# Kernel tuning notes

Measured on AMD Instinct MI355X. Metric: run time of the kernel, lower is better.

Reference implementation:

```python
import jax, jax.numpy as jnp
import numpy as np

IMAGE_SIZE = 512


def setup_inputs() -> dict:
    key = jax.random.key(0)
    k1, k2, k3, k4, k5 = jax.random.split(key, 5)
    B, S, C, P = 64, IMAGE_SIZE, 64, IMAGE_SIZE * IMAGE_SIZE
    x = jax.random.normal(k1, (B, S, S), dtype=jnp.float32)
    pattern_importance = jax.random.uniform(k2, (B, C), dtype=jnp.float32)
    idxx = jax.random.randint(k3, (P,), 0, S)
    idxy = jax.random.randint(k4, (P,), 0, S)
    cluster_id = jax.random.randint(k5, (P,), 0, C)
    return {"x": x, "pattern_importance": pattern_importance,
            "idxx": idxx, "idxy": idxy, "cluster_id": cluster_id}


def reference(x, pattern_importance, idxx, idxy, cluster_id):
    S = IMAGE_SIZE
    # fft2 with zero-pad/crop to (S, S), then shift DC to center
    x_fft = jnp.fft.fftshift(jnp.fft.fft2(x, s=(S, S), axes=(-2, -1)), axes=(-2, -1))
    # mask: ones everywhere, per-cluster importance scattered at clustered freq bins
    B = x.shape[0]
    mask = jnp.ones((B, S, S), dtype=x.dtype)
    # mask[j, idxx, idxy] = pattern_importance[j, cluster_id] for all batches j at once
    mask = mask.at[:, idxx, idxy].set(pattern_importance[:, cluster_id])
    x_reject = x_fft * mask
    x_ifft = jnp.real(jnp.fft.ifft2(jnp.fft.ifftshift(x_reject, axes=(-2, -1)),
                                    s=(x.shape[1], x.shape[2]), axes=(-2, -1)))
    return x_ifft
```

## Files before the change

### kernel.cpp

```cpp
#include <hip/hip_runtime.h>

#define INV_N2 (1.0f/262144.0f)
#define HALF_INV (0.5f*INV_N2)
#define TP 17
#define YT_B ((size_t)(264 * 512))

typedef unsigned u32x2 __attribute__((ext_vector_type(2)));
typedef float v2f __attribute__((ext_vector_type(2)));

__device__ __forceinline__ v2f v2(float a, float b) { v2f r; r.x = a; r.y = b; return r; }
__device__ __forceinline__ int brev9(int v) { return (int)(__brev((unsigned)v) >> 23); }
__device__ __forceinline__ float hsin(float rev) { return __builtin_amdgcn_sinf(rev); }
__device__ __forceinline__ float hcos(float rev) { return __builtin_amdgcn_cosf(rev); }

template<int CTRL>
__device__ __forceinline__ float xdpp(float x) {
  int v = __float_as_int(x);
  return __int_as_float(__builtin_amdgcn_update_dpp(v, v, CTRL, 0xF, 0xF, true));
}
__device__ __forceinline__ float xs1(float x) { return xdpp<0xB1>(x); }
__device__ __forceinline__ float xs2(float x) { return xdpp<0x4E>(x); }
__device__ __forceinline__ float xs8(float x) { return xdpp<0x128>(x); }
__device__ __forceinline__ float xs4(float x) {
  return __int_as_float(__builtin_amdgcn_ds_swizzle(__float_as_int(x), 0x101F));
}
__device__ __forceinline__ void swp16(float x, float &lo, float &hi) {
#if __has_builtin(__builtin_amdgcn_permlane16_swap)
  u32x2 r = __builtin_amdgcn_permlane16_swap(__float_as_uint(x), __float_as_uint(x), false, false);
  lo = __uint_as_float(r[0]); hi = __uint_as_float(r[1]);
#else
  float p = __int_as_float(__builtin_amdgcn_ds_swizzle(__float_as_int(x), 0x401F));
  bool up = (threadIdx.x & 16) != 0;
  lo = up ? p : x; hi = up ? x : p;
#endif
}
__device__ __forceinline__ void swp32(float x, float &lo, float &hi) {
#if __has_builtin(__builtin_amdgcn_permlane32_swap)
  u32x2 r = __builtin_amdgcn_permlane32_swap(__float_as_uint(x), __float_as_uint(x), false, false);
  lo = __uint_as_float(r[0]); hi = __uint_as_float(r[1]);
#else
  float p = __shfl_xor(x, 32, 64);
  bool up = (threadIdx.x & 32) != 0;
  lo = up ? p : x; hi = up ? x : p;
#endif
}

struct Tw { float c[8], s[8]; };
__device__ __forceinline__ Tw make_tw(int lane) {
  Tw t;
  float a0 = (float)lane        * (1.0f/512.0f);
  float a1 = (float)lane        * (1.0f/256.0f);
  float a2 = (float)lane        * (1.0f/128.0f);
  float a3 = (float)(lane & 31) * (1.0f/64.0f);
  float a4 = (float)(lane & 15) * (1.0f/32.0f);
  float a5 = (float)(lane & 7)  * (1.0f/16.0f);
  float a6 = (float)(lane & 3)  * (1.0f/8.0f);
  float a7 = (float)(lane & 1)  * (1.0f/4.0f);
  t.c[0]=hcos(a0); t.s[0]=hsin(a0); t.c[1]=hcos(a1); t.s[1]=hsin(a1);
  t.c[2]=hcos(a2); t.s[2]=hsin(a2); t.c[3]=hcos(a3); t.s[3]=hsin(a3);
  t.c[4]=hcos(a4); t.s[4]=hsin(a4); t.c[5]=hcos(a5); t.s[5]=hsin(a5);
  t.c[6]=hcos(a6); t.s[6]=hsin(a6); t.c[7]=hcos(a7); t.s[7]=hsin(a7);
  return t;
}

#define FWD_PK_XS(S, XCHG, CC, SS) { \
  const bool up = (lane & (S)) != 0; \
  const float sg = up ? -1.0f : 1.0f; \
  const float wr = up ? (CC) : 1.0f; \
  const float wi = up ? -(SS) : 0.0f; \
  const v2f sgv = v2(sg,sg), wrv = v2(wr,wr), wiv = v2(wi,wi); \
  _Pragma("unroll") for (int j = 0; j < 4; ++j) { \
    v2f Rr = v2(XCHG(Xr[j].x), XCHG(Xr[j].y)); \
    v2f Ri = v2(XCHG(Xi[j].x), XCHG(Xi[j].y)); \
    v2f vr = sgv*Xr[j] + Rr; v2f vi = sgv*Xi[j] + Ri; \
    Xr[j] = vr*wrv - vi*wiv; Xi[j] = vr*wiv + vi*wrv; } }

#define FWD_PK_SW(S, SWP, CC, SS) { \
  const bool up = (lane & (S)) != 0; \
  const float sg = up ? -1.0f : 1.0f; \
  const float wr = up ? (CC) : 1.0f; \
  const float wi = up ? -(SS) : 0.0f; \
  const v2f sgv = v2(sg,sg), wrv = v2(wr,wr), wiv = v2(wi,wi); \
  _Pragma("unroll") for (int j = 0; j < 4; ++j) { \
    float l0,h0,l1,h1; \
    SWP(Xr[j].x,l0,h0); SWP(Xr[j].y,l1,h1); \
    v2f Lr = v2(l0,l1), Hr = v2(h0,h1); \
    SWP(Xi[j].x,l0,h0); SWP(Xi[j].y,l1,h1); \
    v2f Li = v2(l0,l1), Hi = v2(h0,h1); \
    v2f vr = sgv*Hr + Lr; v2f vi = sgv*Hi + Li; \
    Xr[j] = vr*wrv - vi*wiv; Xi[j] = vr*wiv + vi*wrv; } }

#define INV_PK_XS(S, XCHG, CC, SS) { \
  const bool up = (lane & (S)) != 0; \
  const float wr = up ? (CC) : 1.0f; \
  const float wi = up ? (SS) : 0.0f; \
  const float sg = up ? -1.0f : 1.0f; \
  const v2f sgv = v2(sg,sg), wrv = v2(wr,wr), wiv = v2(wi,wi); \
  _Pragma("unroll") for (int j = 0; j < 4; ++j) { \
    v2f Zr = Xr[j]*wrv - Xi[j]*wiv; \
    v2f Zi = Xr[j]*wiv + Xi[j]*wrv; \
    v2f Rr = v2(XCHG(Zr.x), XCHG(Zr.y)); \
    v2f Ri = v2(XCHG(Zi.x), XCHG(Zi.y)); \
    Xr[j] = sgv*Zr + Rr; Xi[j] = sgv*Zi + Ri; } }

#define INV_PK_SW(S, SWP, CC, SS) { \
  const bool up = (lane & (S)) != 0; \
  const float wr = up ? (CC) : 1.0f; \
  const float wi = up ? (SS) : 0.0f; \
  const float sg = up ? -1.0f : 1.0f; \
  const v2f sgv = v2(sg,sg), wrv = v2(wr,wr), wiv = v2(wi,wi); \
  _Pragma("unroll") for (int j = 0; j < 4; ++j) { \
    v2f Zr = Xr[j]*wrv - Xi[j]*wiv; \
    v2f Zi = Xr[j]*wiv + Xi[j]*wrv; \
    float l0,h0,l1,h1; \
    SWP(Zr.x,l0,h0); SWP(Zr.y,l1,h1); \
    v2f Lr = v2(l0,l1), Hr = v2(h0,h1); \
    SWP(Zi.x,l0,h0); SWP(Zi.y,l1,h1); \
    v2f Li = v2(l0,l1), Hi = v2(h0,h1); \
    Xr[j] = sgv*Hr + Lr; Xi[j] = sgv*Hi + Li; } }

__device__ __forceinline__ void wave_fft512_fwd(v2f Xr[4], v2f Xi[4], int lane,
                                                const Tw& t) {
  {
    const float c8 = 0.70710678118654752f;
    float wr = t.c[0], wi = -t.s[0];
    float w1r = c8*(wr + wi), w1i = c8*(wi - wr);
    v2f Tr0 = v2(wr, w1r), Ti0 = v2(wi, w1i);
    { v2f Sr = Xr[0]+Xr[2], Si = Xi[0]+Xi[2];
      v2f Dr = Xr[0]-Xr[2], Di = Xi[0]-Xi[2];
      Xr[0] = Sr; Xi[0] = Si;
      Xr[2] = Dr*Tr0 - Di*Ti0; Xi[2] = Dr*Ti0 + Di*Tr0; }
    { v2f Sr = Xr[1]+Xr[3], Si = Xi[1]+Xi[3];
      v2f Dr = Xr[1]-Xr[3], Di = Xi[1]-Xi[3];
      Xr[1] = Sr; Xi[1] = Si;
      Xr[3] = Dr*Ti0 + Di*Tr0; Xi[3] = Di*Ti0 - Dr*Tr0; }
  }
  {
    v2f Tr = v2(t.c[1], -t.s[1]), Ti = v2(-t.s[1], -t.c[1]);
    #pragma unroll
    for (int j = 0; j < 4; j += 2) {
      v2f Sr = Xr[j]+Xr[j+1], Si = Xi[j]+Xi[j+1];
      v2f Dr = Xr[j]-Xr[j+1], Di = Xi[j]-Xi[j+1];
      Xr[j] = Sr; Xi[j] = Si;
      Xr[j+1] = Dr*Tr - Di*Ti; Xi[j+1] = Dr*Ti + Di*Tr;
    }
  }
  {
    float wr = t.c[2], wi = -t.s[2];
    #pragma unroll
    for (int j = 0; j < 4; ++j) {
      float sr = Xr[j].x + Xr[j].y, si = Xi[j].x + Xi[j].y;
      float dr = Xr[j].x - Xr[j].y, di = Xi[j].x - Xi[j].y;
      Xr[j] = v2(sr, dr*wr - di*wi);
      Xi[j] = v2(si, dr*wi + di*wr);
    }
  }
  FWD_PK_SW(32, swp32, t.c[3], t.s[3])
  FWD_PK_SW(16, swp16, t.c[4], t.s[4])
  FWD_PK_XS(8,  xs8,  t.c[5], t.s[5])
  FWD_PK_XS(4,  xs4,  t.c[6], t.s[6])
  FWD_PK_XS(2,  xs2,  t.c[7], t.s[7])
  {
    const float sg = (lane & 1) ? -1.0f : 1.0f;
    const v2f sgv = v2(sg, sg);
    #pragma unroll
    for (int j = 0; j < 4; ++j) {
      v2f Rr = v2(xs1(Xr[j].x), xs1(Xr[j].y));
      v2f Ri = v2(xs1(Xi[j].x), xs1(Xi[j].y));
      Xr[j] = sgv*Xr[j] + Rr; Xi[j] = sgv*Xi[j] + Ri;
    }
  }
}

__device__ __forceinline__ void wave_fft512_inv(v2f Xr[4], v2f Xi[4], int lane,
                                                const Tw& t) {
  {
    const float sg = (lane & 1) ? -1.0f : 1.0f;
    const v2f sgv = v2(sg, sg);
    #pragma unroll
    for (int j = 0; j < 4; ++j) {
      v2f Rr = v2(xs1(Xr[j].x), xs1(Xr[j].y));
      v2f Ri = v2(xs1(Xi[j].x), xs1(Xi[j].y));
      Xr[j] = sgv*Xr[j] + Rr; Xi[j] = sgv*Xi[j] + Ri;
    }
  }
  INV_PK_XS(2,  xs2,  t.c[7], t.s[7])
  INV_PK_XS(4,  xs4,  t.c[6], t.s[6])
  INV_PK_XS(8,  xs8,  t.c[5], t.s[5])
  INV_PK_SW(16, swp16, t.c[4], t.s[4])
  INV_PK_SW(32, swp32, t.c[3], t.s[3])
  {
    float wr = t.c[2], wi = t.s[2];
    #pragma unroll
    for (int j = 0; j < 4; ++j) {
      float tr = Xr[j].y*wr - Xi[j].y*wi, ti = Xr[j].y*wi + Xi[j].y*wr;
      Xr[j] = v2(Xr[j].x + tr, Xr[j].x - tr);
      Xi[j] = v2(Xi[j].x + ti, Xi[j].x - ti);
    }
  }
  {
    v2f Tr = v2(t.c[1], -t.s[1]), Ti = v2(t.s[1], t.c[1]);
    #pragma unroll
    for (int j = 0; j < 4; j += 2) {
      v2f tr = Xr[j+1]*Tr - Xi[j+1]*Ti;
      v2f ti = Xr[j+1]*Ti + Xi[j+1]*Tr;
      Xr[j+1] = Xr[j] - tr; Xi[j+1] = Xi[j] - ti;
      Xr[j]   = Xr[j] + tr; Xi[j]   = Xi[j] + ti;
    }
  }
  {
    const float c8 = 0.70710678118654752f;
    float wr = t.c[0], wi = t.s[0];
    float w1r = c8*(wr - wi), w1i = c8*(wr + wi);
    v2f Tr0 = v2(wr, w1r), Ti0 = v2(wi, w1i);
    { v2f tr = Xr[2]*Tr0 - Xi[2]*Ti0;
      v2f ti = Xr[2]*Ti0 + Xi[2]*Tr0;
      Xr[2] = Xr[0] - tr; Xi[2] = Xi[0] - ti;
      Xr[0] = Xr[0] + tr; Xi[0] = Xi[0] + ti; }
    { v2f tr = Xr[3]*Tr0 + Xi[3]*Ti0;
      v2f ti = Xr[3]*Tr0 - Xi[3]*Ti0;
      tr = -(Xr[3]*Ti0) - Xi[3]*Tr0;
      ti = Xr[3]*Tr0 - Xi[3]*Ti0;
      Xr[3] = Xr[1] - tr; Xi[3] = Xi[1] - ti;
      Xr[1] = Xr[1] + tr; Xi[1] = Xi[1] + ti; }
  }
}

__global__ void k_scatter(const int* __restrict__ idxx, const int* __restrict__ idxy,
                          const int* __restrict__ cid, int* __restrict__ W) {
  int p = blockIdx.x * 256 + threadIdx.x;
  int u = (idxx[p] + 256) & 511;
  int v = (idxy[p] + 256) & 511;
  atomicMax(&W[u * 512 + v], (p << 6) | cid[p]);
}

__global__ void k_pack(const int* __restrict__ W, int* __restrict__ pk) {
  int idx = blockIdx.x * 256 + threadIdx.x;
  if (idx >= 264 * 512) return;
  int j = idx >> 9, n = idx & 511;
  int out = (127 << 7) | 127;
  if (j < 257) {
    int v = (j == 256) ? 256 : brev9(2 * j);
    int u = brev9(n);
    int c1 = W[u * 512 + v];
    int c2 = W[((512 - u) & 511) * 512 + ((512 - v) & 511)];
    int a = (c1 < 0) ? 127 : (c1 & 63);
    int b = (c2 < 0) ? 127 : (c2 & 63);
    out = (b << 7) | a;
  }
  pk[j * 512 + n] = out;
}

__global__ __launch_bounds__(512) void k_fwd_rows(const float* __restrict__ x,
                                                  float2* __restrict__ Yt) {
  __shared__ float sm[2 * 264 * TP];
  float* tR = sm;
  float* tI = sm + 264 * TP;
  int tid = threadIdx.x, w = tid >> 6, lane = tid & 63;
  int R0 = blockIdx.x * 16;
  int bb = R0 >> 9, r0 = R0 & 511;
  const float* rowA = x + (size_t)(R0 + 2 * w) * 512;
  const float* rowB = rowA + 512;
  Tw t = make_tw(lane);
  v2f Xr[4], Xi[4];
  #pragma unroll
  for (int j = 0; j < 4; ++j) {
    Xr[j] = v2(rowA[(2*j)*64 + lane], rowA[(2*j+1)*64 + lane]);
    Xi[j] = v2(rowB[(2*j)*64 + lane], rowB[(2*j+1)*64 + lane]);
  }
  wave_fft512_fwd(Xr, Xi, lane, t);
  float* zr = sm + w * 1024;
  float* zi = zr + 512;
  #pragma unroll
  for (int j = 0; j < 4; ++j) {
    zr[(2*j)*64 + lane] = Xr[j].x; zr[(2*j+1)*64 + lane] = Xr[j].y;
    zi[(2*j)*64 + lane] = Xi[j].x; zi[(2*j+1)*64 + lane] = Xi[j].y;
  }
  float ar[4], ai[4], br[4], bi[4];
  #pragma unroll
  for (int k = 0; k < 4; ++k) {
    int j = k * 64 + lane;
    int n2 = 2 * j;
    int kf = brev9(n2);
    int m = brev9((512 - kf) & 511);
    float er = zr[n2], ei = zi[n2];
    float mr = zr[m],  mi = zi[m];
    ar[k] = 0.5f * (er + mr); ai[k] = 0.5f * (ei - mi);
    br[k] = 0.5f * (ei + mi); bi[k] = 0.5f * (mr - er);
  }
  float a256 = zr[1], b256 = zi[1];
  __syncthreads();
  #pragma unroll
  for (int k = 0; k < 4; ++k) {
    int j = k * 64 + lane;
    tR[j*TP + 2*w]     = ar[k]; tI[j*TP + 2*w]     = ai[k];
    tR[j*TP + 2*w + 1] = br[k]; tI[j*TP + 2*w + 1] = bi[k];
  }
  if (lane == 0) {
    tR[256*TP + 2*w]     = a256; tI[256*TP + 2*w]     = 0.0f;
    tR[256*TP + 2*w + 1] = b256; tI[256*TP + 2*w + 1] = 0.0f;
  }
  __syncthreads();
  #pragma unroll
  for (int rep = 0; rep < 9; ++rep) {
    int e = rep * 512 + tid;
    int j = e >> 4, rr = e & 15;
    if (j < 257)
      Yt[((size_t)bb * 264 + j) * 512 + r0 + rr] =
        make_float2(tR[j*TP + rr], tI[j*TP + rr]);
  }
}

__global__ __launch_bounds__(512) void k_cols(float2* __restrict__ Yt,
                                              const int* __restrict__ pk,
                                              const float* __restrict__ pimp) {
  __shared__ float pilx[128];
  int tid = threadIdx.x;
  int b = blockIdx.x / 33, g = blockIdx.x % 33;
  if (tid < 128) pilx[tid] = (tid < 64) ? pimp[b * 64 + tid] * HALF_INV : HALF_INV;
  int w = tid >> 6, lane = tid & 63;
  int j = g * 8 + w;
  float2* col = Yt + ((size_t)b * 264 + j) * 512;
  const int* cm = pk + j * 512;
  int pcm[8];
  v2f Xr[4], Xi[4];
  #pragma unroll
  for (int q = 0; q < 4; ++q) {
    float2 v0 = col[(2*q)*64 + lane];
    float2 v1 = col[(2*q+1)*64 + lane];
    Xr[q] = v2(v0.x, v1.x); Xi[q] = v2(v0.y, v1.y);
    pcm[2*q]   = cm[(2*q)*64 + lane];
    pcm[2*q+1] = cm[(2*q+1)*64 + lane];
  }
  Tw t = make_tw(lane);
  wave_fft512_fwd(Xr, Xi, lane, t);
  __syncthreads();
  #pragma unroll
  for (int q = 0; q < 4; ++q) {
    int p0 = pcm[2*q], p1 = pcm[2*q+1];
    v2f mv = v2(pilx[p0 & 127] + pilx[(p0 >> 7) & 127],
                pilx[p1 & 127] + pilx[(p1 >> 7) & 127]);
    Xr[q] *= mv; Xi[q] *= mv;
  }
  wave_fft512_inv(Xr, Xi, lane, t);
  #pragma unroll
  for (int q = 0; q < 4; ++q) {
    col[(2*q)*64 + lane]   = make_float2(Xr[q].x, Xi[q].x);
    col[(2*q+1)*64 + lane] = make_float2(Xr[q].y, Xi[q].y);
  }
}

__global__ __launch_bounds__(512) void k_inv_rows(const float2* __restrict__ Yt,
                                                  float* __restrict__ out) {
  __shared__ float tR[264 * TP], tI[264 * TP];
  int tid = threadIdx.x, w = tid >> 6, lane = tid & 63;
  int R0 = blockIdx.x * 16;
  int bb = R0 >> 9, r0 = R0 & 511;
  #pragma unroll
  for (int rep = 0; rep < 9; ++rep) {
    int e = rep * 512 + tid;
    int j = e >> 4, rr = e & 15;
    if (j < 257) {
      float2 v = Yt[((size_t)bb * 264 + j) * 512 + r0 + rr];
      tR[j*TP + rr] = v.x; tI[j*TP + rr] = v.y;
    }
  }
  Tw t = make_tw(lane);
  __syncthreads();
  v2f Xr[4], Xi[4];
  #pragma unroll
  for (int q = 0; q < 4; ++q) {
    float xr2[2], xi2[2];
    #pragma unroll
    for (int h = 0; h < 2; ++h) {
      int n = (2*q + h) * 64 + lane;
      int v9 = brev9(n);
      int j2 = brev9((512 - v9) & 511) >> 1;
      bool oddx = (n & 1) && (n != 1);
      int j = (n & 1) ? ((n == 1) ? 256 : j2) : (n >> 1);
      float s = oddx ? -1.0f : 1.0f;
      float ar = tR[j*TP + 2*w],     ai = tI[j*TP + 2*w];
      float br = tR[j*TP + 2*w + 1], bi = tI[j*TP + 2*w + 1];
      xr2[h] = ar - s * bi;
      xi2[h] = fmaf(s, ai, br);
    }
    Xr[q] = v2(xr2[0], xr2[1]); Xi[q] = v2(xi2[0], xi2[1]);
  }
  wave_fft512_inv(Xr, Xi, lane, t);
  float* orowA = out + (size_t)(R0 + 2 * w) * 512;
  float* orowB = orowA + 512;
  #pragma unroll
  for (int q = 0; q < 4; ++q) {
    orowA[(2*q)*64 + lane]   = Xr[q].x;
    orowA[(2*q+1)*64 + lane] = Xr[q].y;
    orowB[(2*q)*64 + lane]   = Xi[q].x;
    orowB[(2*q+1)*64 + lane] = Xi[q].y;
  }
}

extern "C" void kernel_launch(void* const* d_in, const int* in_sizes, int n_in,
                              void* d_out, int out_size, void* d_ws, size_t ws_size,
                              hipStream_t stream) {
  const float* x    = (const float*)d_in[0];
  const float* pimp = (const float*)d_in[1];
  const int* idxx   = (const int*)d_in[2];
  const int* idxy   = (const int*)d_in[3];
  const int* cid    = (const int*)d_in[4];

  float2* Yt = (float2*)d_ws;
  int* W  = (int*)((char*)d_ws + (size_t)64 * YT_B * sizeof(float2));
  int* pk = W + 512 * 512;

  hipMemsetAsync(W, 0xFF, 512 * 512 * sizeof(int), stream);
  k_scatter  <<<1024, 256, 0, stream>>>(idxx, idxy, cid, W);
  k_pack     <<<(264 * 512 + 255) / 256, 256, 0, stream>>>(W, pk);
  k_fwd_rows <<<2048, 512, 0, stream>>>(x, Yt);
  k_cols     <<<64 * 33, 512, 0, stream>>>(Yt, pk, pimp);
  k_inv_rows <<<2048, 512, 0, stream>>>(Yt, (float*)d_out);
}
```

Before: 199.8 us.

## Emit inverse-row inputs in blocked layout from column kernel, simplify inverse rows

The column FFT kernel now does the real-pair unpacking (using cross-lane swaps) itself and writes its results to a second buffer. That buffer uses a row-group-blocked layout already indexed by the target frequency. The inverse row kernel can then load contiguous float4 tiles and read its inputs straight from shared memory, without the bit-reverse index computation and the strided gather. This is meant to cut uncoalesced global reads and ALU work in the last stage, at the cost of scattered 8-byte writes in the column kernel and a separate workspace region.

```diff
diff --git a/kernel.cpp b/kernel.cpp
--- a/kernel.cpp
+++ b/kernel.cpp
@@ -4,6 +4,7 @@
 #define HALF_INV (0.5f*INV_N2)
 #define TP 17
 #define YT_B ((size_t)(264 * 512))
+#define Y2N 520
 
 typedef unsigned u32x2 __attribute__((ext_vector_type(2)));
 typedef float v2f __attribute__((ext_vector_type(2)));
@@ -217,10 +218,8 @@
       v2f ti = Xr[2]*Ti0 + Xi[2]*Tr0;
       Xr[2] = Xr[0] - tr; Xi[2] = Xi[0] - ti;
       Xr[0] = Xr[0] + tr; Xi[0] = Xi[0] + ti; }
-    { v2f tr = Xr[3]*Tr0 + Xi[3]*Ti0;
+    { v2f tr = -(Xr[3]*Ti0) - Xi[3]*Tr0;
       v2f ti = Xr[3]*Tr0 - Xi[3]*Ti0;
-      tr = -(Xr[3]*Ti0) - Xi[3]*Tr0;
-      ti = Xr[3]*Tr0 - Xi[3]*Ti0;
       Xr[3] = Xr[1] - tr; Xi[3] = Xi[1] - ti;
       Xr[1] = Xr[1] + tr; Xi[1] = Xi[1] + ti; }
   }
@@ -311,7 +310,8 @@
   }
 }
 
-__global__ __launch_bounds__(512) void k_cols(float2* __restrict__ Yt,
+__global__ __launch_bounds__(512) void k_cols(const float2* __restrict__ Yt,
+                                              float2* __restrict__ Yt2,
                                               const int* __restrict__ pk,
                                               const float* __restrict__ pimp) {
   __shared__ float pilx[128];
@@ -320,7 +320,7 @@
   if (tid < 128) pilx[tid] = (tid < 64) ? pimp[b * 64 + tid] * HALF_INV : HALF_INV;
   int w = tid >> 6, lane = tid & 63;
   int j = g * 8 + w;
-  float2* col = Yt + ((size_t)b * 264 + j) * 512;
+  const float2* col = Yt + ((size_t)b * 264 + j) * 512;
   const int* cm = pk + j * 512;
   int pcm[8];
   v2f Xr[4], Xi[4];
@@ -343,51 +343,54 @@
     Xr[q] *= mv; Xi[q] *= mv;
   }
   wave_fft512_inv(Xr, Xi, lane, t);
-  #pragma unroll
-  for (int q = 0; q < 4; ++q) {
-    col[(2*q)*64 + lane]   = make_float2(Xr[q].x, Xi[q].x);
-    col[(2*q+1)*64 + lane] = make_float2(Xr[q].y, Xi[q].y);
-  }
-}
-
-__global__ __launch_bounds__(512) void k_inv_rows(const float2* __restrict__ Yt,
+  if (j <= 256) {
+    int n_e = (j == 256) ? 1 : 2 * j;
+    int n_o = (j >= 1 && j <= 255) ? brev9(512 - brev9(2 * j)) : 513;
+    bool odd = (lane & 1) != 0;
+    int nsel = odd ? n_o : n_e;
+    int rpb = b * 256 + (lane >> 1);
+    #pragma unroll
+    for (int q = 0; q < 4; ++q) {
+      #pragma unroll
+      for (int h = 0; h < 2; ++h) {
+        float xr = h ? Xr[q].y : Xr[q].x;
+        float xi = h ? Xi[q].y : Xi[q].x;
+        float p  = xr - xs1(xi);
+        float s2 = xi + xs1(xr);
+        float ox = odd ? s2 : p;
+        float oy = odd ? p  : s2;
+        int rp = rpb + (2*q + h) * 32;
+        Yt2[((size_t)(rp >> 3) * Y2N + nsel) * 8 + (rp & 7)] = make_float2(ox, oy);
+      }
+    }
+  }
+}
+
+__global__ __launch_bounds__(512) void k_inv_rows(const float2* __restrict__ Yt2,
                                                   float* __restrict__ out) {
-  __shared__ float tR[264 * TP], tI[264 * TP];
+  __shared__ float tR[512 * 9], tI[512 * 9];
   int tid = threadIdx.x, w = tid >> 6, lane = tid & 63;
-  int R0 = blockIdx.x * 16;
-  int bb = R0 >> 9, r0 = R0 & 511;
-  #pragma unroll
-  for (int rep = 0; rep < 9; ++rep) {
-    int e = rep * 512 + tid;
-    int j = e >> 4, rr = e & 15;
-    if (j < 257) {
-      float2 v = Yt[((size_t)bb * 264 + j) * 512 + r0 + rr];
-      tR[j*TP + rr] = v.x; tI[j*TP + rr] = v.y;
-    }
+  int g = blockIdx.x;
+  const float4* src = (const float4*)(Yt2 + (size_t)g * Y2N * 8);
+  #pragma unroll
+  for (int rep = 0; rep < 4; ++rep) {
+    int m = rep * 512 + tid;
+    int n = m >> 2, c = m & 3;
+    float4 v = src[m];
+    tR[n*9 + 2*c]     = v.x; tI[n*9 + 2*c]     = v.y;
+    tR[n*9 + 2*c + 1] = v.z; tI[n*9 + 2*c + 1] = v.w;
   }
   Tw t = make_tw(lane);
   __syncthreads();
   v2f Xr[4], Xi[4];
   #pragma unroll
   for (int q = 0; q < 4; ++q) {
-    float xr2[2], xi2[2];
-    #pragma unroll
-    for (int h = 0; h < 2; ++h) {
-      int n = (2*q + h) * 64 + lane;
-      int v9 = brev9(n);
-      int j2 = brev9((512 - v9) & 511) >> 1;
-      bool oddx = (n & 1) && (n != 1);
-      int j = (n & 1) ? ((n == 1) ? 256 : j2) : (n >> 1);
-      float s = oddx ? -1.0f : 1.0f;
-      float ar = tR[j*TP + 2*w],     ai = tI[j*TP + 2*w];
-      float br = tR[j*TP + 2*w + 1], bi = tI[j*TP + 2*w + 1];
-      xr2[h] = ar - s * bi;
-      xi2[h] = fmaf(s, ai, br);
-    }
-    Xr[q] = v2(xr2[0], xr2[1]); Xi[q] = v2(xi2[0], xi2[1]);
+    int n0 = (2*q)*64 + lane, n1 = (2*q+1)*64 + lane;
+    Xr[q] = v2(tR[n0*9 + w], tR[n1*9 + w]);
+    Xi[q] = v2(tI[n0*9 + w], tI[n1*9 + w]);
   }
   wave_fft512_inv(Xr, Xi, lane, t);
-  float* orowA = out + (size_t)(R0 + 2 * w) * 512;
+  float* orowA = out + (size_t)(g * 16 + 2 * w) * 512;
   float* orowB = orowA + 512;
   #pragma unroll
   for (int q = 0; q < 4; ++q) {
@@ -410,11 +413,12 @@
   float2* Yt = (float2*)d_ws;
   int* W  = (int*)((char*)d_ws + (size_t)64 * YT_B * sizeof(float2));
   int* pk = W + 512 * 512;
+  float2* Yt2 = (float2*)((char*)d_ws + (size_t)72 * 1024 * 1024);
 
   hipMemsetAsync(W, 0xFF, 512 * 512 * sizeof(int), stream);
   k_scatter  <<<1024, 256, 0, stream>>>(idxx, idxy, cid, W);
   k_pack     <<<(264 * 512 + 255) / 256, 256, 0, stream>>>(W, pk);
   k_fwd_rows <<<2048, 512, 0, stream>>>(x, Yt);
-  k_cols     <<<64 * 33, 512, 0, stream>>>(Yt, pk, pimp);
-  k_inv_rows <<<2048, 512, 0, stream>>>(Yt, (float*)d_out);
-}
+  k_cols     <<<64 * 33, 512, 0, stream>>>(Yt, Yt2, pk, pimp);
+  k_inv_rows <<<2048, 512, 0, stream>>>(Yt2, (float*)d_out);
+}
```

After: 209.9 us. +5.0%, slower.

## Process two FFT lines per wave with 256-thread blocks

Applied to the files above, without the earlier changes.

Each wavefront now runs two 512-point FFTs at once (eight packed registers instead of four), and the blocks in the row, column and inverse-row kernels shrink from 512 to 256 threads while covering the same rows or columns. The aim is more instruction-level parallelism per wave and amortised twiddle setup and cross-lane exchange, with fewer waves per block. The cost is higher register pressure, which may lower occupancy, and each remaining thread does more of the shared-memory transpose traffic.

```diff
diff --git a/kernel.cpp b/kernel.cpp
--- a/kernel.cpp
+++ b/kernel.cpp
@@ -69,7 +69,7 @@
   const float wr = up ? (CC) : 1.0f; \
   const float wi = up ? -(SS) : 0.0f; \
   const v2f sgv = v2(sg,sg), wrv = v2(wr,wr), wiv = v2(wi,wi); \
-  _Pragma("unroll") for (int j = 0; j < 4; ++j) { \
+  _Pragma("unroll") for (int j = 0; j < 8; ++j) { \
     v2f Rr = v2(XCHG(Xr[j].x), XCHG(Xr[j].y)); \
     v2f Ri = v2(XCHG(Xi[j].x), XCHG(Xi[j].y)); \
     v2f vr = sgv*Xr[j] + Rr; v2f vi = sgv*Xi[j] + Ri; \
@@ -81,7 +81,7 @@
   const float wr = up ? (CC) : 1.0f; \
   const float wi = up ? -(SS) : 0.0f; \
   const v2f sgv = v2(sg,sg), wrv = v2(wr,wr), wiv = v2(wi,wi); \
-  _Pragma("unroll") for (int j = 0; j < 4; ++j) { \
+  _Pragma("unroll") for (int j = 0; j < 8; ++j) { \
     float l0,h0,l1,h1; \
     SWP(Xr[j].x,l0,h0); SWP(Xr[j].y,l1,h1); \
     v2f Lr = v2(l0,l1), Hr = v2(h0,h1); \
@@ -96,7 +96,7 @@
   const float wi = up ? (SS) : 0.0f; \
   const float sg = up ? -1.0f : 1.0f; \
   const v2f sgv = v2(sg,sg), wrv = v2(wr,wr), wiv = v2(wi,wi); \
-  _Pragma("unroll") for (int j = 0; j < 4; ++j) { \
+  _Pragma("unroll") for (int j = 0; j < 8; ++j) { \
     v2f Zr = Xr[j]*wrv - Xi[j]*wiv; \
     v2f Zi = Xr[j]*wiv + Xi[j]*wrv; \
     v2f Rr = v2(XCHG(Zr.x), XCHG(Zr.y)); \
@@ -109,7 +109,7 @@
   const float wi = up ? (SS) : 0.0f; \
   const float sg = up ? -1.0f : 1.0f; \
   const v2f sgv = v2(sg,sg), wrv = v2(wr,wr), wiv = v2(wi,wi); \
-  _Pragma("unroll") for (int j = 0; j < 4; ++j) { \
+  _Pragma("unroll") for (int j = 0; j < 8; ++j) { \
     v2f Zr = Xr[j]*wrv - Xi[j]*wiv; \
     v2f Zi = Xr[j]*wiv + Xi[j]*wrv; \
     float l0,h0,l1,h1; \
@@ -119,26 +119,29 @@
     v2f Li = v2(l0,l1), Hi = v2(h0,h1); \
     Xr[j] = sgv*Hr + Lr; Xi[j] = sgv*Hi + Li; } }
 
-__device__ __forceinline__ void wave_fft512_fwd(v2f Xr[4], v2f Xi[4], int lane,
-                                                const Tw& t) {
+__device__ __forceinline__ void wave_fft512_fwd2(v2f Xr[8], v2f Xi[8], int lane,
+                                                 const Tw& t) {
   {
     const float c8 = 0.70710678118654752f;
     float wr = t.c[0], wi = -t.s[0];
     float w1r = c8*(wr + wi), w1i = c8*(wi - wr);
     v2f Tr0 = v2(wr, w1r), Ti0 = v2(wi, w1i);
-    { v2f Sr = Xr[0]+Xr[2], Si = Xi[0]+Xi[2];
-      v2f Dr = Xr[0]-Xr[2], Di = Xi[0]-Xi[2];
-      Xr[0] = Sr; Xi[0] = Si;
-      Xr[2] = Dr*Tr0 - Di*Ti0; Xi[2] = Dr*Ti0 + Di*Tr0; }
-    { v2f Sr = Xr[1]+Xr[3], Si = Xi[1]+Xi[3];
-      v2f Dr = Xr[1]-Xr[3], Di = Xi[1]-Xi[3];
-      Xr[1] = Sr; Xi[1] = Si;
-      Xr[3] = Dr*Ti0 + Di*Tr0; Xi[3] = Di*Ti0 - Dr*Tr0; }
+    #pragma unroll
+    for (int o = 0; o < 8; o += 4) {
+      { v2f Sr = Xr[o]+Xr[o+2], Si = Xi[o]+Xi[o+2];
+        v2f Dr = Xr[o]-Xr[o+2], Di = Xi[o]-Xi[o+2];
+        Xr[o] = Sr; Xi[o] = Si;
+        Xr[o+2] = Dr*Tr0 - Di*Ti0; Xi[o+2] = Dr*Ti0 + Di*Tr0; }
+      { v2f Sr = Xr[o+1]+Xr[o+3], Si = Xi[o+1]+Xi[o+3];
+        v2f Dr = Xr[o+1]-Xr[o+3], Di = Xi[o+1]-Xi[o+3];
+        Xr[o+1] = Sr; Xi[o+1] = Si;
+        Xr[o+3] = Dr*Ti0 + Di*Tr0; Xi[o+3] = Di*Ti0 - Dr*Tr0; }
+    }
   }
   {
     v2f Tr = v2(t.c[1], -t.s[1]), Ti = v2(-t.s[1], -t.c[1]);
     #pragma unroll
-    for (int j = 0; j < 4; j += 2) {
+    for (int j = 0; j < 8; j += 2) {
       v2f Sr = Xr[j]+Xr[j+1], Si = Xi[j]+Xi[j+1];
       v2f Dr = Xr[j]-Xr[j+1], Di = Xi[j]-Xi[j+1];
       Xr[j] = Sr; Xi[j] = Si;
@@ -148,7 +151,7 @@
   {
     float wr = t.c[2], wi = -t.s[2];
     #pragma unroll
-    for (int j = 0; j < 4; ++j) {
+    for (int j = 0; j < 8; ++j) {
       float sr = Xr[j].x + Xr[j].y, si = Xi[j].x + Xi[j].y;
       float dr = Xr[j].x - Xr[j].y, di = Xi[j].x - Xi[j].y;
       Xr[j] = v2(sr, dr*wr - di*wi);
@@ -164,7 +167,7 @@
     const float sg = (lane & 1) ? -1.0f : 1.0f;
     const v2f sgv = v2(sg, sg);
     #pragma unroll
-    for (int j = 0; j < 4; ++j) {
+    for (int j = 0; j < 8; ++j) {
       v2f Rr = v2(xs1(Xr[j].x), xs1(Xr[j].y));
       v2f Ri = v2(xs1(Xi[j].x), xs1(Xi[j].y));
       Xr[j] = sgv*Xr[j] + Rr; Xi[j] = sgv*Xi[j] + Ri;
@@ -172,13 +175,13 @@
   }
 }
 
-__device__ __forceinline__ void wave_fft512_inv(v2f Xr[4], v2f Xi[4], int lane,
-                                                const Tw& t) {
+__device__ __forceinline__ void wave_fft512_inv2(v2f Xr[8], v2f Xi[8], int lane,
+                                                 const Tw& t) {
   {
     const float sg = (lane & 1) ? -1.0f : 1.0f;
     const v2f sgv = v2(sg, sg);
     #pragma unroll
-    for (int j = 0; j < 4; ++j) {
+    for (int j = 0; j < 8; ++j) {
       v2f Rr = v2(xs1(Xr[j].x), xs1(Xr[j].y));
       v2f Ri = v2(xs1(Xi[j].x), xs1(Xi[j].y));
       Xr[j] = sgv*Xr[j] + Rr; Xi[j] = sgv*Xi[j] + Ri;
@@ -192,7 +195,7 @@
   {
     float wr = t.c[2], wi = t.s[2];
     #pragma unroll
-    for (int j = 0; j < 4; ++j) {
+    for (int j = 0; j < 8; ++j) {
       float tr = Xr[j].y*wr - Xi[j].y*wi, ti = Xr[j].y*wi + Xi[j].y*wr;
       Xr[j] = v2(Xr[j].x + tr, Xr[j].x - tr);
       Xi[j] = v2(Xi[j].x + ti, Xi[j].x - ti);
@@ -201,7 +204,7 @@
   {
     v2f Tr = v2(t.c[1], -t.s[1]), Ti = v2(t.s[1], t.c[1]);
     #pragma unroll
-    for (int j = 0; j < 4; j += 2) {
+    for (int j = 0; j < 8; j += 2) {
       v2f tr = Xr[j+1]*Tr - Xi[j+1]*Ti;
       v2f ti = Xr[j+1]*Ti + Xi[j+1]*Tr;
       Xr[j+1] = Xr[j] - tr; Xi[j+1] = Xi[j] - ti;
@@ -213,16 +216,17 @@
     float wr = t.c[0], wi = t.s[0];
     float w1r = c8*(wr - wi), w1i = c8*(wr + wi);
     v2f Tr0 = v2(wr, w1r), Ti0 = v2(wi, w1i);
-    { v2f tr = Xr[2]*Tr0 - Xi[2]*Ti0;
-      v2f ti = Xr[2]*Ti0 + Xi[2]*Tr0;
-      Xr[2] = Xr[0] - tr; Xi[2] = Xi[0] - ti;
-      Xr[0] = Xr[0] + tr; Xi[0] = Xi[0] + ti; }
-    { v2f tr = Xr[3]*Tr0 + Xi[3]*Ti0;
-      v2f ti = Xr[3]*Tr0 - Xi[3]*Ti0;
-      tr = -(Xr[3]*Ti0) - Xi[3]*Tr0;
-      ti = Xr[3]*Tr0 - Xi[3]*Ti0;
-      Xr[3] = Xr[1] - tr; Xi[3] = Xi[1] - ti;
-      Xr[1] = Xr[1] + tr; Xi[1] = Xi[1] + ti; }
+    #pragma unroll
+    for (int o = 0; o < 8; o += 4) {
+      { v2f tr = Xr[o+2]*Tr0 - Xi[o+2]*Ti0;
+        v2f ti = Xr[o+2]*Ti0 + Xi[o+2]*Tr0;
+        Xr[o+2] = Xr[o] - tr; Xi[o+2] = Xi[o] - ti;
+        Xr[o]   = Xr[o] + tr; Xi[o]   = Xi[o] + ti; }
+      { v2f tr = -(Xr[o+3]*Ti0) - Xi[o+3]*Tr0;
+        v2f ti = Xr[o+3]*Tr0 - Xi[o+3]*Ti0;
+        Xr[o+3] = Xr[o+1] - tr; Xi[o+3] = Xi[o+1] - ti;
+        Xr[o+1] = Xr[o+1] + tr; Xi[o+1] = Xi[o+1] + ti; }
+    }
   }
 }
 
@@ -251,7 +255,7 @@
   pk[j * 512 + n] = out;
 }
 
-__global__ __launch_bounds__(512) void k_fwd_rows(const float* __restrict__ x,
+__global__ __launch_bounds__(256) void k_fwd_rows(const float* __restrict__ x,
                                                   float2* __restrict__ Yt) {
   __shared__ float sm[2 * 264 * TP];
   float* tR = sm;
@@ -259,51 +263,64 @@
   int tid = threadIdx.x, w = tid >> 6, lane = tid & 63;
   int R0 = blockIdx.x * 16;
   int bb = R0 >> 9, r0 = R0 & 511;
-  const float* rowA = x + (size_t)(R0 + 2 * w) * 512;
-  const float* rowB = rowA + 512;
+  const float* r00 = x + (size_t)(R0 + 4 * w) * 512;
   Tw t = make_tw(lane);
-  v2f Xr[4], Xi[4];
+  v2f Xr[8], Xi[8];
   #pragma unroll
   for (int j = 0; j < 4; ++j) {
-    Xr[j] = v2(rowA[(2*j)*64 + lane], rowA[(2*j+1)*64 + lane]);
-    Xi[j] = v2(rowB[(2*j)*64 + lane], rowB[(2*j+1)*64 + lane]);
-  }
-  wave_fft512_fwd(Xr, Xi, lane, t);
-  float* zr = sm + w * 1024;
-  float* zi = zr + 512;
+    Xr[j]   = v2(r00[(2*j)*64 + lane],        r00[(2*j+1)*64 + lane]);
+    Xi[j]   = v2(r00[512 + (2*j)*64 + lane],  r00[512 + (2*j+1)*64 + lane]);
+    Xr[4+j] = v2(r00[1024 + (2*j)*64 + lane], r00[1024 + (2*j+1)*64 + lane]);
+    Xi[4+j] = v2(r00[1536 + (2*j)*64 + lane], r00[1536 + (2*j+1)*64 + lane]);
+  }
+  wave_fft512_fwd2(Xr, Xi, lane, t);
+  float* zr0 = sm + w * 2048;
+  float* zi0 = zr0 + 512;
+  float* zr1 = zr0 + 1024;
+  float* zi1 = zr0 + 1536;
   #pragma unroll
   for (int j = 0; j < 4; ++j) {
-    zr[(2*j)*64 + lane] = Xr[j].x; zr[(2*j+1)*64 + lane] = Xr[j].y;
-    zi[(2*j)*64 + lane] = Xi[j].x; zi[(2*j+1)*64 + lane] = Xi[j].y;
-  }
-  float ar[4], ai[4], br[4], bi[4];
+    zr0[(2*j)*64 + lane] = Xr[j].x;   zr0[(2*j+1)*64 + lane] = Xr[j].y;
+    zi0[(2*j)*64 + lane] = Xi[j].x;   zi0[(2*j+1)*64 + lane] = Xi[j].y;
+    zr1[(2*j)*64 + lane] = Xr[4+j].x; zr1[(2*j+1)*64 + lane] = Xr[4+j].y;
+    zi1[(2*j)*64 + lane] = Xi[4+j].x; zi1[(2*j+1)*64 + lane] = Xi[4+j].y;
+  }
+  float ar0[4], ai0[4], br0[4], bi0[4];
+  float ar1[4], ai1[4], br1[4], bi1[4];
   #pragma unroll
   for (int k = 0; k < 4; ++k) {
     int j = k * 64 + lane;
     int n2 = 2 * j;
     int kf = brev9(n2);
     int m = brev9((512 - kf) & 511);
-    float er = zr[n2], ei = zi[n2];
-    float mr = zr[m],  mi = zi[m];
-    ar[k] = 0.5f * (er + mr); ai[k] = 0.5f * (ei - mi);
-    br[k] = 0.5f * (ei + mi); bi[k] = 0.5f * (mr - er);
-  }
-  float a256 = zr[1], b256 = zi[1];
+    float er = zr0[n2], ei = zi0[n2], mr = zr0[m], mi = zi0[m];
+    ar0[k] = 0.5f*(er + mr); ai0[k] = 0.5f*(ei - mi);
+    br0[k] = 0.5f*(ei + mi); bi0[k] = 0.5f*(mr - er);
+    float er1 = zr1[n2], ei1 = zi1[n2], mr1 = zr1[m], mi1 = zi1[m];
+    ar1[k] = 0.5f*(er1 + mr1); ai1[k] = 0.5f*(ei1 - mi1);
+    br1[k] = 0.5f*(ei1 + mi1); bi1[k] = 0.5f*(mr1 - er1);
+  }
+  float a256_0 = zr0[1], b256_0 = zi0[1];
+  float a256_1 = zr1[1], b256_1 = zi1[1];
   __syncthreads();
   #pragma unroll
   for (int k = 0; k < 4; ++k) {
     int j = k * 64 + lane;
-    tR[j*TP + 2*w]     = ar[k]; tI[j*TP + 2*w]     = ai[k];
-    tR[j*TP + 2*w + 1] = br[k]; tI[j*TP + 2*w + 1] = bi[k];
+    tR[j*TP + 4*w]     = ar0[k]; tI[j*TP + 4*w]     = ai0[k];
+    tR[j*TP + 4*w + 1] = br0[k]; tI[j*TP + 4*w + 1] = bi0[k];
+    tR[j*TP + 4*w + 2] = ar1[k]; tI[j*TP + 4*w + 2] = ai1[k];
+    tR[j*TP + 4*w + 3] = br1[k]; tI[j*TP + 4*w + 3] = bi1[k];
   }
   if (lane == 0) {
-    tR[256*TP + 2*w]     = a256; tI[256*TP + 2*w]     = 0.0f;
-    tR[256*TP + 2*w + 1] = b256; tI[256*TP + 2*w + 1] = 0.0f;
+    tR[256*TP + 4*w]     = a256_0; tI[256*TP + 4*w]     = 0.0f;
+    tR[256*TP + 4*w + 1] = b256_0; tI[256*TP + 4*w + 1] = 0.0f;
+    tR[256*TP + 4*w + 2] = a256_1; tI[256*TP + 4*w + 2] = 0.0f;
+    tR[256*TP + 4*w + 3] = b256_1; tI[256*TP + 4*w + 3] = 0.0f;
   }
   __syncthreads();
   #pragma unroll
-  for (int rep = 0; rep < 9; ++rep) {
-    int e = rep * 512 + tid;
+  for (int rep = 0; rep < 17; ++rep) {
+    int e = rep * 256 + tid;
     int j = e >> 4, rr = e & 15;
     if (j < 257)
       Yt[((size_t)bb * 264 + j) * 512 + r0 + rr] =
@@ -311,7 +328,7 @@
   }
 }
 
-__global__ __launch_bounds__(512) void k_cols(float2* __restrict__ Yt,
+__global__ __launch_bounds__(256) void k_cols(float2* __restrict__ Yt,
                                               const int* __restrict__ pk,
                                               const float* __restrict__ pimp) {
   __shared__ float pilx[128];
@@ -319,46 +336,53 @@
   int b = blockIdx.x / 33, g = blockIdx.x % 33;
   if (tid < 128) pilx[tid] = (tid < 64) ? pimp[b * 64 + tid] * HALF_INV : HALF_INV;
   int w = tid >> 6, lane = tid & 63;
-  int j = g * 8 + w;
-  float2* col = Yt + ((size_t)b * 264 + j) * 512;
-  const int* cm = pk + j * 512;
-  int pcm[8];
-  v2f Xr[4], Xi[4];
+  int j0 = g * 8 + 2 * w;
+  float2* col0 = Yt + ((size_t)b * 264 + j0) * 512;
+  float2* col1 = col0 + 512;
+  const int* cm0 = pk + j0 * 512;
+  const int* cm1 = cm0 + 512;
+  int pcm[16];
+  v2f Xr[8], Xi[8];
   #pragma unroll
   for (int q = 0; q < 4; ++q) {
-    float2 v0 = col[(2*q)*64 + lane];
-    float2 v1 = col[(2*q+1)*64 + lane];
-    Xr[q] = v2(v0.x, v1.x); Xi[q] = v2(v0.y, v1.y);
-    pcm[2*q]   = cm[(2*q)*64 + lane];
-    pcm[2*q+1] = cm[(2*q+1)*64 + lane];
+    float2 a0 = col0[(2*q)*64 + lane], a1 = col0[(2*q+1)*64 + lane];
+    float2 b0 = col1[(2*q)*64 + lane], b1 = col1[(2*q+1)*64 + lane];
+    Xr[q]   = v2(a0.x, a1.x); Xi[q]   = v2(a0.y, a1.y);
+    Xr[4+q] = v2(b0.x, b1.x); Xi[4+q] = v2(b0.y, b1.y);
+    pcm[2*q]     = cm0[(2*q)*64 + lane];
+    pcm[2*q+1]   = cm0[(2*q+1)*64 + lane];
+    pcm[8+2*q]   = cm1[(2*q)*64 + lane];
+    pcm[8+2*q+1] = cm1[(2*q+1)*64 + lane];
   }
   Tw t = make_tw(lane);
-  wave_fft512_fwd(Xr, Xi, lane, t);
+  wave_fft512_fwd2(Xr, Xi, lane, t);
   __syncthreads();
   #pragma unroll
-  for (int q = 0; q < 4; ++q) {
+  for (int q = 0; q < 8; ++q) {
     int p0 = pcm[2*q], p1 = pcm[2*q+1];
     v2f mv = v2(pilx[p0 & 127] + pilx[(p0 >> 7) & 127],
                 pilx[p1 & 127] + pilx[(p1 >> 7) & 127]);
     Xr[q] *= mv; Xi[q] *= mv;
   }
-  wave_fft512_inv(Xr, Xi, lane, t);
+  wave_fft512_inv2(Xr, Xi, lane, t);
   #pragma unroll
   for (int q = 0; q < 4; ++q) {
-    col[(2*q)*64 + lane]   = make_float2(Xr[q].x, Xi[q].x);
-    col[(2*q+1)*64 + lane] = make_float2(Xr[q].y, Xi[q].y);
-  }
-}
-
-__global__ __launch_bounds__(512) void k_inv_rows(const float2* __restrict__ Yt,
+    col0[(2*q)*64 + lane]   = make_float2(Xr[q].x, Xi[q].x);
+    col0[(2*q+1)*64 + lane] = make_float2(Xr[q].y, Xi[q].y);
+    col1[(2*q)*64 + lane]   = make_float2(Xr[4+q].x, Xi[4+q].x);
+    col1[(2*q+1)*64 + lane] = make_float2(Xr[4+q].y, Xi[4+q].y);
+  }
+}
+
+__global__ __launch_bounds__(256) void k_inv_rows(const float2* __restrict__ Yt,
                                                   float* __restrict__ out) {
   __shared__ float tR[264 * TP], tI[264 * TP];
   int tid = threadIdx.x, w = tid >> 6, lane = tid & 63;
   int R0 = blockIdx.x * 16;
   int bb = R0 >> 9, r0 = R0 & 511;
   #pragma unroll
-  for (int rep = 0; rep < 9; ++rep) {
-    int e = rep * 512 + tid;
+  for (int rep = 0; rep < 17; ++rep) {
+    int e = rep * 256 + tid;
     int j = e >> 4, rr = e & 15;
     if (j < 257) {
       float2 v = Yt[((size_t)bb * 264 + j) * 512 + r0 + rr];
@@ -367,10 +391,10 @@
   }
   Tw t = make_tw(lane);
   __syncthreads();
-  v2f Xr[4], Xi[4];
+  v2f Xr[8], Xi[8];
   #pragma unroll
   for (int q = 0; q < 4; ++q) {
-    float xr2[2], xi2[2];
+    float xr0[2], xi0[2], xr1[2], xi1[2];
     #pragma unroll
     for (int h = 0; h < 2; ++h) {
       int n = (2*q + h) * 64 + lane;
@@ -379,22 +403,27 @@
       bool oddx = (n & 1) && (n != 1);
       int j = (n & 1) ? ((n == 1) ? 256 : j2) : (n >> 1);
       float s = oddx ? -1.0f : 1.0f;
-      float ar = tR[j*TP + 2*w],     ai = tI[j*TP + 2*w];
-      float br = tR[j*TP + 2*w + 1], bi = tI[j*TP + 2*w + 1];
-      xr2[h] = ar - s * bi;
-      xi2[h] = fmaf(s, ai, br);
-    }
-    Xr[q] = v2(xr2[0], xr2[1]); Xi[q] = v2(xi2[0], xi2[1]);
-  }
-  wave_fft512_inv(Xr, Xi, lane, t);
-  float* orowA = out + (size_t)(R0 + 2 * w) * 512;
-  float* orowB = orowA + 512;
+      float ar = tR[j*TP + 4*w],     ai = tI[j*TP + 4*w];
+      float br = tR[j*TP + 4*w + 1], bi = tI[j*TP + 4*w + 1];
+      xr0[h] = ar - s * bi;  xi0[h] = fmaf(s, ai, br);
+      float ar1 = tR[j*TP + 4*w + 2], ai1 = tI[j*TP + 4*w + 2];
+      float br1 = tR[j*TP + 4*w + 3], bi1 = tI[j*TP + 4*w + 3];
+      xr1[h] = ar1 - s * bi1; xi1[h] = fmaf(s, ai1, br1);
+    }
+    Xr[q]   = v2(xr0[0], xr0[1]); Xi[q]   = v2(xi0[0], xi0[1]);
+    Xr[4+q] = v2(xr1[0], xr1[1]); Xi[4+q] = v2(xi1[0], xi1[1]);
+  }
+  wave_fft512_inv2(Xr, Xi, lane, t);
+  float* orA0 = out + (size_t)(R0 + 4 * w) * 512;
+  float* orB0 = orA0 + 512;
+  float* orA1 = orA0 + 1024;
+  float* orB1 = orA0 + 1536;
   #pragma unroll
   for (int q = 0; q < 4; ++q) {
-    orowA[(2*q)*64 + lane]   = Xr[q].x;
-    orowA[(2*q+1)*64 + lane] = Xr[q].y;
-    orowB[(2*q)*64 + lane]   = Xi[q].x;
-    orowB[(2*q+1)*64 + lane] = Xi[q].y;
+    orA0[(2*q)*64 + lane]   = Xr[q].x;   orA0[(2*q+1)*64 + lane] = Xr[q].y;
+    orB0[(2*q)*64 + lane]   = Xi[q].x;   orB0[(2*q+1)*64 + lane] = Xi[q].y;
+    orA1[(2*q)*64 + lane]   = Xr[4+q].x; orA1[(2*q+1)*64 + lane] = Xr[4+q].y;
+    orB1[(2*q)*64 + lane]   = Xi[4+q].x; orB1[(2*q+1)*64 + lane] = Xi[4+q].y;
   }
 }
 
@@ -414,7 +443,7 @@
   hipMemsetAsync(W, 0xFF, 512 * 512 * sizeof(int), stream);
   k_scatter  <<<1024, 256, 0, stream>>>(idxx, idxy, cid, W);
   k_pack     <<<(264 * 512 + 255) / 256, 256, 0, stream>>>(W, pk);
-  k_fwd_rows <<<2048, 512, 0, stream>>>(x, Yt);
-  k_cols     <<<64 * 33, 512, 0, stream>>>(Yt, pk, pimp);
-  k_inv_rows <<<2048, 512, 0, stream>>>(Yt, (float*)d_out);
-}
+  k_fwd_rows <<<2048, 256, 0, stream>>>(x, Yt);
+  k_cols     <<<64 * 33, 256, 0, stream>>>(Yt, pk, pimp);
+  k_inv_rows <<<2048, 256, 0, stream>>>(Yt, (float*)d_out);
+}
```

New measurement: 196.0 us. About the same (-1.9%).
